# Kernel optimization log

Hardware: AMD Instinct MI355X
Metric: run time of the kernel (lower is better)

The kernel has to match this reference:

```python
import jax, jax.numpy as jnp
import numpy as np

N, E, DIN, H, C = 50000, 800000, 128, 2, 64  # C = hidden_dim*heads (per-head out channels); concat=False -> mean over heads -> layer out dim C
NUM_CLASSES = 4
EPS_GN = 1e-5


def setup_inputs() -> dict:
    key = jax.random.key(0)

    def rn(i, shape, scale):
        return (jax.random.normal(jax.random.fold_in(key, i), shape) * scale).astype(jnp.float32)

    inp = {
        "x": rn(0, (N, DIN), 1.0),
        "edge_index": jax.random.randint(jax.random.fold_in(key, 1), (2, E), 0, N, dtype=jnp.int32),
    }
    layer_in = [DIN, C]
    for li, din in enumerate(layer_in, 1):
        s = 1.0 / np.sqrt(din)
        base = 10 * li
        inp[f"Wl{li}"] = rn(base + 0, (din, H * C), s)
        inp[f"bl{li}"] = jnp.zeros((H * C,), jnp.float32)
        inp[f"Wr{li}"] = rn(base + 1, (din, H * C), s)
        inp[f"br{li}"] = jnp.zeros((H * C,), jnp.float32)
        inp[f"att{li}"] = rn(base + 2, (H, C), 1.0 / np.sqrt(C))
        inp[f"bias{li}"] = jnp.zeros((C,), jnp.float32)
        inp[f"gng{li}"] = jnp.ones((C,), jnp.float32)   # GraphNorm weight
        inp[f"gnb{li}"] = jnp.zeros((C,), jnp.float32)  # GraphNorm bias
        inp[f"gna{li}"] = jnp.ones((C,), jnp.float32)   # GraphNorm mean_scale
    inp["W1"] = rn(100, (C, NUM_CLASSES), 1.0 / np.sqrt(C))
    inp["b1"] = jnp.zeros((NUM_CLASSES,), jnp.float32)
    return inp


def gatv2_layer(x, src, dst, Wl, bl, Wr, br, att, bias):
    # PyG GATv2Conv, concat=False. x: [N, din]
    n = x.shape[0]
    xl = (x @ Wl + bl).reshape(n, H, C)  # source transform
    xr = (x @ Wr + br).reshape(n, H, C)  # target transform
    m = jax.nn.leaky_relu(xl[src] + xr[dst], negative_slope=0.2)  # [E', H, C]
    e = jnp.einsum('ehc,hc->eh', m, att)                           # [E', H]
    emax = jax.lax.stop_gradient(jax.ops.segment_max(e, dst, num_segments=n))
    ee = jnp.exp(e - emax[dst])
    denom = jax.ops.segment_sum(ee, dst, num_segments=n)
    alpha = ee / (denom[dst] + 1e-16)                              # softmax over in-edges of each target
    out = jax.ops.segment_sum(alpha[:, :, None] * xl[src], dst, num_segments=n)  # [N, H, C]
    return out.mean(axis=1) + bias  # concat=False -> mean over heads


def graph_norm(x, gamma, beta, mean_scale):
    # single-graph GraphNorm: stats over all nodes, per feature
    mean = x.mean(axis=0, keepdims=True)
    xc = x - mean_scale * mean
    var = (xc * xc).mean(axis=0, keepdims=True)
    return gamma * xc * jax.lax.rsqrt(var + EPS_GN) + beta


def reference(x, edge_index,
              Wl1, bl1, Wr1, br1, att1, bias1, gng1, gnb1, gna1,
              Wl2, bl2, Wr2, br2, att2, bias2, gng2, gnb2, gna2,
              W1, b1):
    src, dst = edge_index[0], edge_index[1]
    loops = jnp.arange(N, dtype=src.dtype)  # add_self_loops=True
    src = jnp.concatenate([src, loops])
    dst = jnp.concatenate([dst, loops])

    h = gatv2_layer(x, src, dst, Wl1, bl1, Wr1, br1, att1, bias1)
    h = graph_norm(h, gng1, gnb1, gna1)
    h = gatv2_layer(h, src, dst, Wl2, bl2, Wr2, br2, att2, bias2)
    h = graph_norm(h, gng2, gnb2, gna2)

    logits = h @ W1 + b1  # dropout is identity in eval
    return jax.nn.log_softmax(logits, axis=1)
```

## Files before the change

kernel.cpp:

```cpp
#include <hip/hip_runtime.h>
#include <hip/hip_bf16.h>
#include <math.h>

#define HC   128
#define CCH  64
#define NBK  256

typedef __attribute__((ext_vector_type(8))) short short8;
typedef __attribute__((ext_vector_type(4))) float floatx4;

__device__ __forceinline__ unsigned short f2bf(float f) {
  unsigned u = __float_as_uint(f);
  u += 0x7fffu + ((u >> 16) & 1u);
  return (unsigned short)(u >> 16);
}

__device__ __forceinline__ void unpack8(uint4 u, float* f) {
  f[0] = __uint_as_float(u.x << 16);
  f[1] = __uint_as_float(u.x & 0xffff0000u);
  f[2] = __uint_as_float(u.y << 16);
  f[3] = __uint_as_float(u.y & 0xffff0000u);
  f[4] = __uint_as_float(u.z << 16);
  f[5] = __uint_as_float(u.z & 0xffff0000u);
  f[6] = __uint_as_float(u.w << 16);
  f[7] = __uint_as_float(u.w & 0xffff0000u);
}

template <int CTRL>
__device__ __forceinline__ float dpp_add(float x) {
  int t = __builtin_amdgcn_update_dpp(0, __float_as_int(x), CTRL, 0xf, 0xf, true);
  return x + __int_as_float(t);
}

template <int K>
__device__ __forceinline__ void gemm32rows(
    const unsigned short* __restrict__ A,
    const unsigned short* __restrict__ Wlt, const unsigned short* __restrict__ Wrt,
    const float* __restrict__ bl, const float* __restrict__ br,
    unsigned short* __restrict__ xlb, unsigned short* __restrict__ xrb,
    int M, int row0, int tid) {
  const int w = tid >> 6;
  const int lane = tid & 63;
  const bool isR = w >= 2;
  const unsigned short* Wt = isR ? Wrt : Wlt;
  const float* bias = isR ? br : bl;
  unsigned short* out = isR ? xrb : xlb;
  const int col0 = (w & 1) * 64;
  const int mrow = lane & 15, quad = lane >> 4;
  const unsigned short* pa0 = A + (size_t)(row0 + mrow) * K + quad * 8;
  const unsigned short* pa1 = pa0 + (size_t)16 * K;
  const unsigned short* pb = Wt + (size_t)(col0 + mrow) * K + quad * 8;
  floatx4 acc[2][4];
#pragma unroll
  for (int gp = 0; gp < 2; gp++)
#pragma unroll
    for (int ct = 0; ct < 4; ct++) acc[gp][ct] = (floatx4){0.f, 0.f, 0.f, 0.f};
#pragma unroll
  for (int k0 = 0; k0 < K; k0 += 32) {
    short8 a0 = *(const short8*)(pa0 + k0);
    short8 a1 = *(const short8*)(pa1 + k0);
    short8 b0 = *(const short8*)(pb + k0);
    short8 b1 = *(const short8*)(pb + 16 * K + k0);
    short8 b2 = *(const short8*)(pb + 32 * K + k0);
    short8 b3 = *(const short8*)(pb + 48 * K + k0);
    acc[0][0] = __builtin_amdgcn_mfma_f32_16x16x32_bf16(a0, b0, acc[0][0], 0, 0, 0);
    acc[1][0] = __builtin_amdgcn_mfma_f32_16x16x32_bf16(a1, b0, acc[1][0], 0, 0, 0);
    acc[0][1] = __builtin_amdgcn_mfma_f32_16x16x32_bf16(a0, b1, acc[0][1], 0, 0, 0);
    acc[1][1] = __builtin_amdgcn_mfma_f32_16x16x32_bf16(a1, b1, acc[1][1], 0, 0, 0);
    acc[0][2] = __builtin_amdgcn_mfma_f32_16x16x32_bf16(a0, b2, acc[0][2], 0, 0, 0);
    acc[1][2] = __builtin_amdgcn_mfma_f32_16x16x32_bf16(a1, b2, acc[1][2], 0, 0, 0);
    acc[0][3] = __builtin_amdgcn_mfma_f32_16x16x32_bf16(a0, b3, acc[0][3], 0, 0, 0);
    acc[1][3] = __builtin_amdgcn_mfma_f32_16x16x32_bf16(a1, b3, acc[1][3], 0, 0, 0);
  }
#pragma unroll
  for (int gp = 0; gp < 2; gp++) {
#pragma unroll
    for (int ct = 0; ct < 4; ct++) {
      int col = col0 + ct * 16 + mrow;
      float bv = bias[col];
#pragma unroll
      for (int r = 0; r < 4; r++) {
        int row = row0 + gp * 16 + quad * 4 + r;
        if (row < M) out[(size_t)row * HC + col] = f2bf(acc[gp][ct][r] + bv);
      }
    }
  }
}

__global__ __launch_bounds__(256) void bin_cast(
    const int* __restrict__ ei, int E, int chunk, int nB,
    int* __restrict__ blkCnt, int* __restrict__ bucketTotal,
    const float* __restrict__ x, unsigned short* __restrict__ xb, int cnt4,
    const float* __restrict__ Wl, const float* __restrict__ Wr,
    unsigned short* __restrict__ Wlt, unsigned short* __restrict__ Wrt) {
  if ((int)blockIdx.x < NBK) {
    __shared__ int cnt[512];
    for (int j = threadIdx.x; j < nB; j += 256) cnt[j] = 0;
    __syncthreads();
    int e0 = blockIdx.x * chunk;
    int e1 = e0 + chunk; e1 = e1 < E ? e1 : E;
    int e = e0 + threadIdx.x;
    for (; e + 768 < e1; e += 1024) {
      int d0 = __builtin_nontemporal_load(ei + E + e);
      int d1 = __builtin_nontemporal_load(ei + E + e + 256);
      int d2 = __builtin_nontemporal_load(ei + E + e + 512);
      int d3 = __builtin_nontemporal_load(ei + E + e + 768);
      atomicAdd(&cnt[d0 >> 7], 1);
      atomicAdd(&cnt[d1 >> 7], 1);
      atomicAdd(&cnt[d2 >> 7], 1);
      atomicAdd(&cnt[d3 >> 7], 1);
    }
    for (; e < e1; e += 256) {
      int dst = __builtin_nontemporal_load(ei + E + e);
      atomicAdd(&cnt[dst >> 7], 1);
    }
    __syncthreads();
    for (int j = threadIdx.x; j < nB; j += 256) {
      int c = cnt[j];
      blkCnt[blockIdx.x * nB + j] = c;
      if (c) atomicAdd(&bucketTotal[j], c);
    }
  } else {
    int gid = (blockIdx.x - NBK) * 256 + threadIdx.x;
    if (gid < 32768) {
      int sel = gid >> 14;
      int i = gid & 16383;
      int nn = i >> 7, k = i & 127;
      const float* W = sel ? Wr : Wl;
      unsigned short* Wt = sel ? Wrt : Wlt;
      Wt[i] = f2bf(W[k * HC + nn]);
    }
    if (gid >= cnt4) return;
    float4 v = ((const float4*)x)[gid];
    ushort4 o;
    o.x = f2bf(v.x); o.y = f2bf(v.y); o.z = f2bf(v.z); o.w = f2bf(v.w);
    ((ushort4*)xb)[gid] = o;
  }
}

__global__ __launch_bounds__(256) void scan_offsets(
    const int* __restrict__ bucketTotal, int* __restrict__ bucketBase,
    int* __restrict__ blkCnt, int nB, int E) {
  const int j = blockIdx.x;
  const int tid = threadIdx.x;
  __shared__ int red[256];
  __shared__ int col[NBK];
  int s = 0;
  for (int k = tid; k < j; k += 256) s += bucketTotal[k];
  red[tid] = s;
  __syncthreads();
  for (int off = 128; off > 0; off >>= 1) {
    if (tid < off) red[tid] += red[tid + off];
    __syncthreads();
  }
  const int base_j = red[0];
  if (tid == 0) {
    bucketBase[j] = base_j;
    if (j == 0) bucketBase[nB] = E;
  }
  int v = 0;
  if (tid < NBK) { v = blkCnt[tid * nB + j]; col[tid] = v; }
  __syncthreads();
  for (int off = 1; off < NBK; off <<= 1) {
    int t = 0;
    if (tid < NBK && tid >= off) t = col[tid - off];
    __syncthreads();
    if (tid < NBK) col[tid] += t;
    __syncthreads();
  }
  if (tid < NBK) blkCnt[tid * nB + j] = base_j + col[tid] - v;
}

__global__ __launch_bounds__(256) void place_gemm1(
    const int* __restrict__ ei, int E, int chunk, int nB,
    const int* __restrict__ blkCnt, unsigned* __restrict__ ebuf,
    const unsigned short* __restrict__ A,
    const unsigned short* __restrict__ Wlt, const unsigned short* __restrict__ Wrt,
    const float* __restrict__ bl, const float* __restrict__ br,
    unsigned short* __restrict__ xlb, unsigned short* __restrict__ xrb, int M) {
  if ((int)blockIdx.x < NBK) {
    __shared__ int cur[512];
    for (int j = threadIdx.x; j < nB; j += 256)
      cur[j] = blkCnt[blockIdx.x * nB + j];
    __syncthreads();
    int e0 = blockIdx.x * chunk;
    int e1 = e0 + chunk; e1 = e1 < E ? e1 : E;
    int e = e0 + threadIdx.x;
    for (; e + 768 < e1; e += 1024) {
      int d0 = __builtin_nontemporal_load(ei + E + e);
      int d1 = __builtin_nontemporal_load(ei + E + e + 256);
      int d2 = __builtin_nontemporal_load(ei + E + e + 512);
      int d3 = __builtin_nontemporal_load(ei + E + e + 768);
      int s0 = __builtin_nontemporal_load(ei + e);
      int s1 = __builtin_nontemporal_load(ei + e + 256);
      int s2 = __builtin_nontemporal_load(ei + e + 512);
      int s3 = __builtin_nontemporal_load(ei + e + 768);
      int p0 = atomicAdd(&cur[d0 >> 7], 1);
      int p1 = atomicAdd(&cur[d1 >> 7], 1);
      int p2 = atomicAdd(&cur[d2 >> 7], 1);
      int p3 = atomicAdd(&cur[d3 >> 7], 1);
      ebuf[p0] = (unsigned)s0 | ((unsigned)(d0 & 127) << 16);
      ebuf[p1] = (unsigned)s1 | ((unsigned)(d1 & 127) << 16);
      ebuf[p2] = (unsigned)s2 | ((unsigned)(d2 & 127) << 16);
      ebuf[p3] = (unsigned)s3 | ((unsigned)(d3 & 127) << 16);
    }
    for (; e < e1; e += 256) {
      int dst = __builtin_nontemporal_load(ei + E + e);
      int src = __builtin_nontemporal_load(ei + e);
      int pos = atomicAdd(&cur[dst >> 7], 1);
      ebuf[pos] = (unsigned)src | ((unsigned)(dst & 127) << 16);
    }
  } else {
    const int row0 = (blockIdx.x - NBK) * 32;
    if (row0 >= M) return;
    gemm32rows<128>(A, Wlt, Wrt, bl, br, xlb, xrb, M, row0, threadIdx.x);
  }
}

__global__ __launch_bounds__(256) void csr_build(
    const unsigned* __restrict__ ebuf, const int* __restrict__ bucketBase,
    int* __restrict__ row_start, int* __restrict__ deg,
    int* __restrict__ csr_src, int N, int EPtot) {
  const int b = blockIdx.x;
  const int tid = threadIdx.x;
  const int node0 = b * 128;
  const int nb = (N - node0) < 128 ? (N - node0) : 128;
  const int ebase = bucketBase[b];
  const int eend = bucketBase[b + 1];
  __shared__ int degL[128], scanL[128], curL[128];
  if (tid < 128) degL[tid] = 0;
  __syncthreads();
  for (int e = ebase + tid; e < eend; e += 256)
    atomicAdd(&degL[(ebuf[e] >> 16) & 127], 1);
  __syncthreads();
  if (tid < 128) scanL[tid] = degL[tid];
  __syncthreads();
  for (int off = 1; off < 128; off <<= 1) {
    int t = 0;
    if (tid < 128 && tid >= off) t = scanL[tid - off];
    __syncthreads();
    if (tid < 128) scanL[tid] += t;
    __syncthreads();
  }
  if (tid < 128) {
    int rs = ebase + (scanL[tid] - degL[tid]) + node0 + tid;
    curL[tid] = rs;
    if (tid < nb) {
      row_start[node0 + tid] = rs;
      deg[node0 + tid] = degL[tid];
    }
  }
  __syncthreads();
  for (int e = ebase + tid; e < eend; e += 256) {
    unsigned p = ebuf[e];
    int pos = atomicAdd(&curL[(p >> 16) & 127], 1);
    csr_src[pos] = (int)(p & 0xffffu);
  }
  __syncthreads();
  if (tid < nb) csr_src[curL[tid]] = node0 + tid;
  if (b == 0 && tid < 32) csr_src[EPtot + tid] = 0;
}

template <int K>
__global__ __launch_bounds__(256) void gemm_mfma(
    const unsigned short* __restrict__ A,
    const unsigned short* __restrict__ Wlt, const unsigned short* __restrict__ Wrt,
    const float* __restrict__ bl, const float* __restrict__ br,
    unsigned short* __restrict__ xlb, unsigned short* __restrict__ xrb, int M) {
  const int row0 = blockIdx.x * 32;
  if (row0 >= M) return;
  gemm32rows<K>(A, Wlt, Wrt, bl, br, xlb, xrb, M, row0, threadIdx.x);
}

__global__ __launch_bounds__(256) void node_attn(
    const unsigned short* __restrict__ xlb, const unsigned short* __restrict__ xrb,
    const int* __restrict__ csr_src, const int* __restrict__ row_start,
    const int* __restrict__ deg, const float* __restrict__ att,
    const float* __restrict__ bias, unsigned short* __restrict__ outb, int n) {
  int wave = (blockIdx.x * blockDim.x + threadIdx.x) >> 6;
  if (wave >= n) return;
  const int node = wave;
  const int lane = threadIdx.x & 63;
  const int g = lane >> 4;
  const int hl = lane & 15;
  const int c8 = hl << 3;

  float r[8], a[8];
  {
    uint4 u = *(const uint4*)(xrb + (size_t)node * HC + c8);
    unpack8(u, r);
    float4 a0 = *(const float4*)(att + c8);
    float4 a1 = *(const float4*)(att + c8 + 4);
    const float L2E = 1.44269504f;
    a[0] = a0.x * L2E; a[1] = a0.y * L2E; a[2] = a0.z * L2E; a[3] = a0.w * L2E;
    a[4] = a1.x * L2E; a[5] = a1.y * L2E; a[6] = a1.z * L2E; a[7] = a1.w * L2E;
  }

  const int p0 = row_start[node];
  const int pend = p0 + deg[node] + 1;

  float d = 0.f;
  float acc[8] = {0.f, 0.f, 0.f, 0.f, 0.f, 0.f, 0.f, 0.f};

  int s0 = __builtin_nontemporal_load(csr_src + p0 + g);
  uint4 A0 = *(const uint4*)(xlb + (size_t)s0 * HC + c8);
  int s1 = __builtin_nontemporal_load(csr_src + p0 + 4 + g);
  uint4 A1 = *(const uint4*)(xlb + (size_t)s1 * HC + c8);
  int s2 = __builtin_nontemporal_load(csr_src + p0 + 8 + g);
  uint4 A2 = *(const uint4*)(xlb + (size_t)s2 * HC + c8);

  for (int p = p0; p < pend; p += 4) {
    int s3 = __builtin_nontemporal_load(csr_src + p + 12 + g);
    uint4 A3 = *(const uint4*)(xlb + (size_t)s3 * HC + c8);

    float v[8];
    unpack8(A0, v);
    float e1 = 0.f, e2 = 0.f;
#pragma unroll
    for (int i = 0; i < 8; i++) {
      float s = v[i] + r[i];
      e1 = fmaf(a[i], s, e1);
      e2 = fmaf(a[i], fabsf(s), e2);
    }
    float e = fmaf(0.4f, e2, 0.6f * e1);
    e = dpp_add<0xB1>(e);
    e = dpp_add<0x4E>(e);
    e = dpp_add<0x141>(e);

    bool valid = (p + g) < pend;
    float w = valid ? exp2f(e) : 0.f;
    d += w;
#pragma unroll
    for (int i = 0; i < 8; i++) acc[i] = fmaf(w, v[i], acc[i]);
    A0 = A1; A1 = A2; A2 = A3;
  }

#pragma unroll
  for (int ofs = 16; ofs <= 32; ofs <<= 1) {
    d += __shfl_xor(d, ofs);
#pragma unroll
    for (int i = 0; i < 8; i++) acc[i] += __shfl_xor(acc[i], ofs);
  }
  float inv = 1.f / (d + 1e-16f);
  const float* bb = bias + (c8 & 63);
  float o[8];
#pragma unroll
  for (int i = 0; i < 8; i++) {
    float t = acc[i] * inv;
    float t2 = __shfl_xor(t, 8);
    o[i] = 0.5f * (t + t2) + bb[i];
  }
  if (lane < 8) {
    uint4 ou;
    ou.x = (unsigned)f2bf(o[0]) | ((unsigned)f2bf(o[1]) << 16);
    ou.y = (unsigned)f2bf(o[2]) | ((unsigned)f2bf(o[3]) << 16);
    ou.z = (unsigned)f2bf(o[4]) | ((unsigned)f2bf(o[5]) << 16);
    ou.w = (unsigned)f2bf(o[6]) | ((unsigned)f2bf(o[7]) << 16);
    *(uint4*)(outb + (size_t)node * CCH + c8) = ou;
  }
}

__global__ __launch_bounds__(256) void gn_stats(
    const unsigned short* __restrict__ y, float* __restrict__ S, int n) {
  __shared__ float l1a[256], l1b[256], l2a[256], l2b[256];
  int half = threadIdx.x & 31;
  int sub = threadIdx.x >> 5;
  float s1a = 0.f, s1b = 0.f, s2a = 0.f, s2b = 0.f;
  int stride = gridDim.x * 8;
  for (int r = blockIdx.x * 8 + sub; r < n; r += stride) {
    unsigned u = ((const unsigned*)(y + (size_t)r * CCH))[half];
    float va = __uint_as_float(u << 16);
    float vb = __uint_as_float(u & 0xffff0000u);
    s1a += va; s2a = fmaf(va, va, s2a);
    s1b += vb; s2b = fmaf(vb, vb, s2b);
  }
  l1a[threadIdx.x] = s1a; l1b[threadIdx.x] = s1b;
  l2a[threadIdx.x] = s2a; l2b[threadIdx.x] = s2b;
  __syncthreads();
  if (threadIdx.x < 32) {
#pragma unroll
    for (int k = 1; k < 8; k++) {
      s1a += l1a[threadIdx.x + 32 * k];
      s1b += l1b[threadIdx.x + 32 * k];
      s2a += l2a[threadIdx.x + 32 * k];
      s2b += l2b[threadIdx.x + 32 * k];
    }
    atomicAdd(&S[2 * half], s1a);
    atomicAdd(&S[2 * half + 1], s1b);
    atomicAdd(&S[64 + 2 * half], s2a);
    atomicAdd(&S[64 + 2 * half + 1], s2b);
  }
}

__global__ __launch_bounds__(256) void gn_stats_prep(
    const unsigned short* __restrict__ y, float* __restrict__ S,
    int* __restrict__ done, const float* __restrict__ gamma,
    const float* __restrict__ beta, const float* __restrict__ mscale,
    const float* __restrict__ Wl2, const float* __restrict__ bl2,
    const float* __restrict__ Wr2, const float* __restrict__ br2,
    unsigned short* __restrict__ Wl2tb, float* __restrict__ bl2p,
    unsigned short* __restrict__ Wr2tb, float* __restrict__ br2p, int n) {
  __shared__ float l1a[256], l1b[256], l2a[256], l2b[256];
  int half = threadIdx.x & 31;
  int sub = threadIdx.x >> 5;
  float s1a = 0.f, s1b = 0.f, s2a = 0.f, s2b = 0.f;
  int stride = gridDim.x * 8;
  for (int r = blockIdx.x * 8 + sub; r < n; r += stride) {
    unsigned u = ((const unsigned*)(y + (size_t)r * CCH))[half];
    float va = __uint_as_float(u << 16);
    float vb = __uint_as_float(u & 0xffff0000u);
    s1a += va; s2a = fmaf(va, va, s2a);
    s1b += vb; s2b = fmaf(vb, vb, s2b);
  }
  l1a[threadIdx.x] = s1a; l1b[threadIdx.x] = s1b;
  l2a[threadIdx.x] = s2a; l2b[threadIdx.x] = s2b;
  __syncthreads();
  if (threadIdx.x < 32) {
#pragma unroll
    for (int k = 1; k < 8; k++) {
      s1a += l1a[threadIdx.x + 32 * k];
      s1b += l1b[threadIdx.x + 32 * k];
      s2a += l2a[threadIdx.x + 32 * k];
      s2b += l2b[threadIdx.x + 32 * k];
    }
    atomicAdd(&S[2 * half], s1a);
    atomicAdd(&S[2 * half + 1], s1b);
    atomicAdd(&S[64 + 2 * half], s2a);
    atomicAdd(&S[64 + 2 * half + 1], s2b);
  }
  __threadfence();
  __shared__ int isLast;
  if (threadIdx.x == 0) {
    int old = atomicAdd(done, 1);
    isLast = (old == (int)gridDim.x - 1) ? 1 : 0;
  }
  __syncthreads();
  if (!isLast) return;
  __threadfence();
  __shared__ float As[64], Bs[64];
  int t = threadIdx.x;
  if (t < 64) {
    float invn = 1.f / (float)n;
    float mu = S[t] * invn;
    float ms = mscale[t];
    float var = S[64 + t] * invn - 2.f * ms * mu * mu + ms * ms * mu * mu;
    float A = gamma[t] * rsqrtf(var + 1e-5f);
    As[t] = A;
    Bs[t] = beta[t] - A * ms * mu;
  }
  __syncthreads();
  const int side = t >> 7, col = t & 127;
  const float* W = side ? Wr2 : Wl2;
  unsigned short* Wt = side ? Wr2tb : Wl2tb;
  const float* bin = side ? br2 : bl2;
  float* bout = side ? br2p : bl2p;
  float s = 0.f;
  for (int c = 0; c < 64; c++) {
    float w = W[c * HC + col];
    Wt[col * 64 + c] = f2bf(As[c] * w);
    s = fmaf(Bs[c], w, s);
  }
  bout[col] = bin[col] + s;
}

__global__ __launch_bounds__(256) void classify(
    const unsigned short* __restrict__ h,
    const float* __restrict__ S, const float* __restrict__ gamma,
    const float* __restrict__ beta, const float* __restrict__ mscale,
    const float* __restrict__ W, const float* __restrict__ b,
    float* __restrict__ out, int n) {
  __shared__ float4 sW[64];
  __shared__ float sBt[256];
  __shared__ float sb[4];
  int tid = threadIdx.x;
  if (tid < 64) {
    float invn = 1.f / (float)n;
    float mu = S[tid] * invn;
    float ms = mscale[tid];
    float var = S[64 + tid] * invn - 2.f * ms * mu * mu + ms * ms * mu * mu;
    float A = gamma[tid] * rsqrtf(var + 1e-5f);
    float B = beta[tid] - A * ms * mu;
    float4 w = ((const float4*)W)[tid];
    sW[tid] = make_float4(A * w.x, A * w.y, A * w.z, A * w.w);
    sBt[tid * 4 + 0] = B * w.x; sBt[tid * 4 + 1] = B * w.y;
    sBt[tid * 4 + 2] = B * w.z; sBt[tid * 4 + 3] = B * w.w;
  }
  __syncthreads();
  if (tid < 4) {
    float s = b[tid];
    for (int c = 0; c < 64; c++) s += sBt[c * 4 + tid];
    sb[tid] = s;
  }
  __syncthreads();
  int node = blockIdx.x * 256 + tid;
  if (node >= n) return;
  float acc0 = sb[0], acc1 = sb[1], acc2 = sb[2], acc3 = sb[3];
  const uint4* row = (const uint4*)(h + (size_t)node * CCH);
#pragma unroll
  for (int k4 = 0; k4 < 8; k4++) {
    uint4 u = row[k4];
    float v[8];
    unpack8(u, v);
#pragma unroll
    for (int j = 0; j < 8; j++) {
      float4 w = sW[k4 * 8 + j];
      acc0 = fmaf(v[j], w.x, acc0);
      acc1 = fmaf(v[j], w.y, acc1);
      acc2 = fmaf(v[j], w.z, acc2);
      acc3 = fmaf(v[j], w.w, acc3);
    }
  }
  float mx = fmaxf(fmaxf(acc0, acc1), fmaxf(acc2, acc3));
  float s = __expf(acc0 - mx) + __expf(acc1 - mx) + __expf(acc2 - mx) + __expf(acc3 - mx);
  float lse = mx + logf(s);
  float4 o = make_float4(acc0 - lse, acc1 - lse, acc2 - lse, acc3 - lse);
  *((float4*)(out + (size_t)node * 4)) = o;
}

extern "C" void kernel_launch(void* const* d_in, const int* in_sizes, int n_in,
                              void* d_out, int out_size, void* d_ws, size_t ws_size,
                              hipStream_t stream) {
  const float* x     = (const float*)d_in[0];
  const int*   ei    = (const int*)d_in[1];
  const float* Wl1   = (const float*)d_in[2];
  const float* bl1   = (const float*)d_in[3];
  const float* Wr1   = (const float*)d_in[4];
  const float* br1   = (const float*)d_in[5];
  const float* att1  = (const float*)d_in[6];
  const float* bias1 = (const float*)d_in[7];
  const float* gng1  = (const float*)d_in[8];
  const float* gnb1  = (const float*)d_in[9];
  const float* gna1  = (const float*)d_in[10];
  const float* Wl2   = (const float*)d_in[11];
  const float* bl2   = (const float*)d_in[12];
  const float* Wr2   = (const float*)d_in[13];
  const float* br2   = (const float*)d_in[14];
  const float* att2  = (const float*)d_in[15];
  const float* bias2 = (const float*)d_in[16];
  const float* gng2  = (const float*)d_in[17];
  const float* gnb2  = (const float*)d_in[18];
  const float* gna2  = (const float*)d_in[19];
  const float* W1    = (const float*)d_in[20];
  const float* b1    = (const float*)d_in[21];

  const int N = in_sizes[0] / 128;
  const int E = in_sizes[1] / 2;
  const int EP = E + N;
  const int nB = (N + 127) >> 7;
  const int chunk = (E + NBK - 1) / NBK;

  int* bucketTotal = (int*)d_ws;
  float* S1  = (float*)(bucketTotal + 512);
  float* S2  = S1 + 128;
  int* done  = (int*)(S2 + 128);
  float* bl2p = (float*)(done + 64);
  float* br2p = bl2p + 128;
  unsigned short* xb    = (unsigned short*)(br2p + 128);
  unsigned short* xlb   = xb + (size_t)N * HC;
  unsigned short* xrb   = xlb + (size_t)N * HC;
  unsigned short* aggb  = xrb + (size_t)N * HC;
  unsigned short* Wl1tb = aggb + (size_t)N * CCH;
  unsigned short* Wr1tb = Wl1tb + HC * HC;
  unsigned short* Wl2tb = Wr1tb + HC * HC;
  unsigned short* Wr2tb = Wl2tb + HC * CCH;
  int* bucketBase = (int*)(Wr2tb + HC * CCH);
  int* blkCnt  = bucketBase + 512 + 8;
  int* row_st  = blkCnt + NBK * 512;
  int* deg     = row_st + N;
  unsigned* ebuf = (unsigned*)(deg + N);
  int* csr_src = (int*)(ebuf + E);

  dim3 b256(256);
  const int gNode = (N * 64 + 255) / 256;
  const int gCls  = (N + 255) / 256;
  const int gCast = (N * 32 + 255) / 256;
  const int gGemm = (N + 31) / 32;

  hipMemsetAsync(d_ws, 0, 4096, stream);

  bin_cast<<<NBK + gCast, b256, 0, stream>>>(
      ei, E, chunk, nB, blkCnt, bucketTotal,
      x, xb, N * 32, Wl1, Wr1, Wl1tb, Wr1tb);

  scan_offsets<<<nB, b256, 0, stream>>>(bucketTotal, bucketBase, blkCnt, nB, E);

  place_gemm1<<<NBK + gGemm, b256, 0, stream>>>(
      ei, E, chunk, nB, blkCnt, ebuf,
      xb, Wl1tb, Wr1tb, bl1, br1, xlb, xrb, N);

  csr_build<<<nB, b256, 0, stream>>>(ebuf, bucketBase, row_st, deg, csr_src, N, EP);

  node_attn<<<gNode, b256, 0, stream>>>(xlb, xrb, csr_src, row_st, deg, att1, bias1, aggb, N);
  gn_stats_prep<<<256, b256, 0, stream>>>(aggb, S1, done, gng1, gnb1, gna1,
                                          Wl2, bl2, Wr2, br2,
                                          Wl2tb, bl2p, Wr2tb, br2p, N);

  gemm_mfma<64><<<gGemm, b256, 0, stream>>>(aggb, Wl2tb, Wr2tb, bl2p, br2p, xlb, xrb, N);
  node_attn<<<gNode, b256, 0, stream>>>(xlb, xrb, csr_src, row_st, deg, att2, bias2, aggb, N);
  gn_stats<<<256, b256, 0, stream>>>(aggb, S2, N);

  classify<<<gCls, b256, 0, stream>>>(aggb, S2, gng2, gnb2, gna2, W1, b1,
                                      (float*)d_out, N);
}
```

Before: 327.0 us.

## Merge edge binning and placement into one pass with fixed-capacity buckets

Edge bucketing now reserves each block's slots per bucket with a global atomicAdd right after the local count, then places edges into fixed-capacity per-bucket regions within the same kernel. This removes the separate offset-scan kernel and lets the CSR build run alongside the first GEMM in one launch, cutting the pipeline from four launches to two. Each CSR block computes its own global base by summing the bucket counts before it. The cost is a second read of edge_index in the binning kernel, plain cached loads instead of nontemporal ones, and a fixed capacity of twice the average bucket size, which would overflow silently on skewed degree distributions.

```diff
diff --git a/kernel.cpp b/kernel.cpp
--- a/kernel.cpp
+++ b/kernel.cpp
@@ -4,7 +4,7 @@
 
 #define HC   128
 #define CCH  64
-#define NBK  256
+#define NBKE 256
 
 typedef __attribute__((ext_vector_type(8))) short short8;
 typedef __attribute__((ext_vector_type(4))) float floatx4;
@@ -87,13 +87,13 @@
   }
 }
 
-__global__ __launch_bounds__(256) void bin_cast(
-    const int* __restrict__ ei, int E, int chunk, int nB,
-    int* __restrict__ blkCnt, int* __restrict__ bucketTotal,
+__global__ __launch_bounds__(256) void binplace_cast(
+    const int* __restrict__ ei, int E, int chunk, int nB, int cap,
+    int* __restrict__ gCnt, unsigned* __restrict__ ebuf,
     const float* __restrict__ x, unsigned short* __restrict__ xb, int cnt4,
     const float* __restrict__ Wl, const float* __restrict__ Wr,
     unsigned short* __restrict__ Wlt, unsigned short* __restrict__ Wrt) {
-  if ((int)blockIdx.x < NBK) {
+  if ((int)blockIdx.x < NBKE) {
     __shared__ int cnt[512];
     for (int j = threadIdx.x; j < nB; j += 256) cnt[j] = 0;
     __syncthreads();
@@ -101,27 +101,50 @@
     int e1 = e0 + chunk; e1 = e1 < E ? e1 : E;
     int e = e0 + threadIdx.x;
     for (; e + 768 < e1; e += 1024) {
-      int d0 = __builtin_nontemporal_load(ei + E + e);
-      int d1 = __builtin_nontemporal_load(ei + E + e + 256);
-      int d2 = __builtin_nontemporal_load(ei + E + e + 512);
-      int d3 = __builtin_nontemporal_load(ei + E + e + 768);
+      int d0 = ei[E + e];
+      int d1 = ei[E + e + 256];
+      int d2 = ei[E + e + 512];
+      int d3 = ei[E + e + 768];
       atomicAdd(&cnt[d0 >> 7], 1);
       atomicAdd(&cnt[d1 >> 7], 1);
       atomicAdd(&cnt[d2 >> 7], 1);
       atomicAdd(&cnt[d3 >> 7], 1);
     }
-    for (; e < e1; e += 256) {
-      int dst = __builtin_nontemporal_load(ei + E + e);
-      atomicAdd(&cnt[dst >> 7], 1);
-    }
+    for (; e < e1; e += 256) atomicAdd(&cnt[ei[E + e] >> 7], 1);
     __syncthreads();
     for (int j = threadIdx.x; j < nB; j += 256) {
       int c = cnt[j];
-      blkCnt[blockIdx.x * nB + j] = c;
-      if (c) atomicAdd(&bucketTotal[j], c);
+      int base = c ? atomicAdd(&gCnt[j], c) : 0;
+      cnt[j] = j * cap + base;
+    }
+    __syncthreads();
+    e = e0 + threadIdx.x;
+    for (; e + 768 < e1; e += 1024) {
+      int d0 = ei[E + e];
+      int d1 = ei[E + e + 256];
+      int d2 = ei[E + e + 512];
+      int d3 = ei[E + e + 768];
+      int s0 = ei[e];
+      int s1 = ei[e + 256];
+      int s2 = ei[e + 512];
+      int s3 = ei[e + 768];
+      int p0 = atomicAdd(&cnt[d0 >> 7], 1);
+      int p1 = atomicAdd(&cnt[d1 >> 7], 1);
+      int p2 = atomicAdd(&cnt[d2 >> 7], 1);
+      int p3 = atomicAdd(&cnt[d3 >> 7], 1);
+      ebuf[p0] = (unsigned)s0 | ((unsigned)(d0 & 127) << 16);
+      ebuf[p1] = (unsigned)s1 | ((unsigned)(d1 & 127) << 16);
+      ebuf[p2] = (unsigned)s2 | ((unsigned)(d2 & 127) << 16);
+      ebuf[p3] = (unsigned)s3 | ((unsigned)(d3 & 127) << 16);
+    }
+    for (; e < e1; e += 256) {
+      int dst = ei[E + e];
+      int src = ei[e];
+      int pos = atomicAdd(&cnt[dst >> 7], 1);
+      ebuf[pos] = (unsigned)src | ((unsigned)(dst & 127) << 16);
     }
   } else {
-    int gid = (blockIdx.x - NBK) * 256 + threadIdx.x;
+    int gid = (blockIdx.x - NBKE) * 256 + threadIdx.x;
     if (gid < 32768) {
       int sel = gid >> 14;
       int i = gid & 16383;
@@ -138,127 +161,68 @@
   }
 }
 
-__global__ __launch_bounds__(256) void scan_offsets(
-    const int* __restrict__ bucketTotal, int* __restrict__ bucketBase,
-    int* __restrict__ blkCnt, int nB, int E) {
-  const int j = blockIdx.x;
-  const int tid = threadIdx.x;
-  __shared__ int red[256];
-  __shared__ int col[NBK];
-  int s = 0;
-  for (int k = tid; k < j; k += 256) s += bucketTotal[k];
-  red[tid] = s;
-  __syncthreads();
-  for (int off = 128; off > 0; off >>= 1) {
-    if (tid < off) red[tid] += red[tid + off];
-    __syncthreads();
-  }
-  const int base_j = red[0];
-  if (tid == 0) {
-    bucketBase[j] = base_j;
-    if (j == 0) bucketBase[nB] = E;
-  }
-  int v = 0;
-  if (tid < NBK) { v = blkCnt[tid * nB + j]; col[tid] = v; }
-  __syncthreads();
-  for (int off = 1; off < NBK; off <<= 1) {
-    int t = 0;
-    if (tid < NBK && tid >= off) t = col[tid - off];
-    __syncthreads();
-    if (tid < NBK) col[tid] += t;
-    __syncthreads();
-  }
-  if (tid < NBK) blkCnt[tid * nB + j] = base_j + col[tid] - v;
-}
-
-__global__ __launch_bounds__(256) void place_gemm1(
-    const int* __restrict__ ei, int E, int chunk, int nB,
-    const int* __restrict__ blkCnt, unsigned* __restrict__ ebuf,
+__global__ __launch_bounds__(256) void csr_gemm1(
+    const unsigned* __restrict__ ebuf, const int* __restrict__ gCnt, int cap,
+    int* __restrict__ row_start, int* __restrict__ deg,
+    int* __restrict__ csr_src, int N, int EPtot, int nB,
     const unsigned short* __restrict__ A,
     const unsigned short* __restrict__ Wlt, const unsigned short* __restrict__ Wrt,
     const float* __restrict__ bl, const float* __restrict__ br,
     unsigned short* __restrict__ xlb, unsigned short* __restrict__ xrb, int M) {
-  if ((int)blockIdx.x < NBK) {
-    __shared__ int cur[512];
-    for (int j = threadIdx.x; j < nB; j += 256)
-      cur[j] = blkCnt[blockIdx.x * nB + j];
-    __syncthreads();
-    int e0 = blockIdx.x * chunk;
-    int e1 = e0 + chunk; e1 = e1 < E ? e1 : E;
-    int e = e0 + threadIdx.x;
-    for (; e + 768 < e1; e += 1024) {
-      int d0 = __builtin_nontemporal_load(ei + E + e);
-      int d1 = __builtin_nontemporal_load(ei + E + e + 256);
-      int d2 = __builtin_nontemporal_load(ei + E + e + 512);
-      int d3 = __builtin_nontemporal_load(ei + E + e + 768);
-      int s0 = __builtin_nontemporal_load(ei + e);
-      int s1 = __builtin_nontemporal_load(ei + e + 256);
-      int s2 = __builtin_nontemporal_load(ei + e + 512);
-      int s3 = __builtin_nontemporal_load(ei + e + 768);
-      int p0 = atomicAdd(&cur[d0 >> 7], 1);
-      int p1 = atomicAdd(&cur[d1 >> 7], 1);
-      int p2 = atomicAdd(&cur[d2 >> 7], 1);
-      int p3 = atomicAdd(&cur[d3 >> 7], 1);
-      ebuf[p0] = (unsigned)s0 | ((unsigned)(d0 & 127) << 16);
-      ebuf[p1] = (unsigned)s1 | ((unsigned)(d1 & 127) << 16);
-      ebuf[p2] = (unsigned)s2 | ((unsigned)(d2 & 127) << 16);
-      ebuf[p3] = (unsigned)s3 | ((unsigned)(d3 & 127) << 16);
-    }
-    for (; e < e1; e += 256) {
-      int dst = __builtin_nontemporal_load(ei + E + e);
-      int src = __builtin_nontemporal_load(ei + e);
-      int pos = atomicAdd(&cur[dst >> 7], 1);
-      ebuf[pos] = (unsigned)src | ((unsigned)(dst & 127) << 16);
-    }
+  if ((int)blockIdx.x < nB) {
+    const int b = blockIdx.x;
+    const int tid = threadIdx.x;
+    __shared__ int red[256];
+    __shared__ int degL[128], scanL[128], curL[128];
+    int s = 0;
+    for (int k = tid; k < b; k += 256) s += gCnt[k];
+    red[tid] = s;
+    __syncthreads();
+    for (int off = 128; off > 0; off >>= 1) {
+      if (tid < off) red[tid] += red[tid + off];
+      __syncthreads();
+    }
+    const int ebase = red[0];
+    const int cnt = gCnt[b];
+    const int node0 = b * 128;
+    const int nb2 = (N - node0) < 128 ? (N - node0) : 128;
+    const unsigned* eb = ebuf + (size_t)b * cap;
+    if (tid < 128) degL[tid] = 0;
+    __syncthreads();
+    for (int e = tid; e < cnt; e += 256)
+      atomicAdd(&degL[(eb[e] >> 16) & 127], 1);
+    __syncthreads();
+    if (tid < 128) scanL[tid] = degL[tid];
+    __syncthreads();
+    for (int off = 1; off < 128; off <<= 1) {
+      int t = 0;
+      if (tid < 128 && tid >= off) t = scanL[tid - off];
+      __syncthreads();
+      if (tid < 128) scanL[tid] += t;
+      __syncthreads();
+    }
+    if (tid < 128) {
+      int rs = ebase + (scanL[tid] - degL[tid]) + node0 + tid;
+      curL[tid] = rs;
+      if (tid < nb2) {
+        row_start[node0 + tid] = rs;
+        deg[node0 + tid] = degL[tid];
+      }
+    }
+    __syncthreads();
+    for (int e = tid; e < cnt; e += 256) {
+      unsigned p = eb[e];
+      int pos = atomicAdd(&curL[(p >> 16) & 127], 1);
+      csr_src[pos] = (int)(p & 0xffffu);
+    }
+    __syncthreads();
+    if (tid < nb2) csr_src[curL[tid]] = node0 + tid;
+    if (b == 0 && tid < 32) csr_src[EPtot + tid] = 0;
   } else {
-    const int row0 = (blockIdx.x - NBK) * 32;
+    const int row0 = (blockIdx.x - nB) * 32;
     if (row0 >= M) return;
     gemm32rows<128>(A, Wlt, Wrt, bl, br, xlb, xrb, M, row0, threadIdx.x);
   }
-}
-
-__global__ __launch_bounds__(256) void csr_build(
-    const unsigned* __restrict__ ebuf, const int* __restrict__ bucketBase,
-    int* __restrict__ row_start, int* __restrict__ deg,
-    int* __restrict__ csr_src, int N, int EPtot) {
-  const int b = blockIdx.x;
-  const int tid = threadIdx.x;
-  const int node0 = b * 128;
-  const int nb = (N - node0) < 128 ? (N - node0) : 128;
-  const int ebase = bucketBase[b];
-  const int eend = bucketBase[b + 1];
-  __shared__ int degL[128], scanL[128], curL[128];
-  if (tid < 128) degL[tid] = 0;
-  __syncthreads();
-  for (int e = ebase + tid; e < eend; e += 256)
-    atomicAdd(&degL[(ebuf[e] >> 16) & 127], 1);
-  __syncthreads();
-  if (tid < 128) scanL[tid] = degL[tid];
-  __syncthreads();
-  for (int off = 1; off < 128; off <<= 1) {
-    int t = 0;
-    if (tid < 128 && tid >= off) t = scanL[tid - off];
-    __syncthreads();
-    if (tid < 128) scanL[tid] += t;
-    __syncthreads();
-  }
-  if (tid < 128) {
-    int rs = ebase + (scanL[tid] - degL[tid]) + node0 + tid;
-    curL[tid] = rs;
-    if (tid < nb) {
-      row_start[node0 + tid] = rs;
-      deg[node0 + tid] = degL[tid];
-    }
-  }
-  __syncthreads();
-  for (int e = ebase + tid; e < eend; e += 256) {
-    unsigned p = ebuf[e];
-    int pos = atomicAdd(&curL[(p >> 16) & 127], 1);
-    csr_src[pos] = (int)(p & 0xffffu);
-  }
-  __syncthreads();
-  if (tid < nb) csr_src[curL[tid]] = node0 + tid;
-  if (b == 0 && tid < 32) csr_src[EPtot + tid] = 0;
 }
 
 template <int K>
@@ -547,10 +511,11 @@
   const int E = in_sizes[1] / 2;
   const int EP = E + N;
   const int nB = (N + 127) >> 7;
-  const int chunk = (E + NBK - 1) / NBK;
-
-  int* bucketTotal = (int*)d_ws;
-  float* S1  = (float*)(bucketTotal + 512);
+  const int chunk = (E + NBKE - 1) / NBKE;
+  const int cap = ((E / nB) * 2 + 255) & ~255;
+
+  int* gCnt = (int*)d_ws;
+  float* S1  = (float*)(gCnt + 512);
   float* S2  = S1 + 128;
   int* done  = (int*)(S2 + 128);
   float* bl2p = (float*)(done + 64);
@@ -563,12 +528,10 @@
   unsigned short* Wr1tb = Wl1tb + HC * HC;
   unsigned short* Wl2tb = Wr1tb + HC * HC;
   unsigned short* Wr2tb = Wl2tb + HC * CCH;
-  int* bucketBase = (int*)(Wr2tb + HC * CCH);
-  int* blkCnt  = bucketBase + 512 + 8;
-  int* row_st  = blkCnt + NBK * 512;
+  int* row_st  = (int*)(Wr2tb + HC * CCH);
   int* deg     = row_st + N;
   unsigned* ebuf = (unsigned*)(deg + N);
-  int* csr_src = (int*)(ebuf + E);
+  int* csr_src = (int*)(ebuf + (size_t)nB * cap);
 
   dim3 b256(256);
   const int gNode = (N * 64 + 255) / 256;
@@ -578,17 +541,13 @@
 
   hipMemsetAsync(d_ws, 0, 4096, stream);
 
-  bin_cast<<<NBK + gCast, b256, 0, stream>>>(
-      ei, E, chunk, nB, blkCnt, bucketTotal,
+  binplace_cast<<<NBKE + gCast, b256, 0, stream>>>(
+      ei, E, chunk, nB, cap, gCnt, ebuf,
       x, xb, N * 32, Wl1, Wr1, Wl1tb, Wr1tb);
 
-  scan_offsets<<<nB, b256, 0, stream>>>(bucketTotal, bucketBase, blkCnt, nB, E);
-
-  place_gemm1<<<NBK + gGemm, b256, 0, stream>>>(
-      ei, E, chunk, nB, blkCnt, ebuf,
+  csr_gemm1<<<nB + gGemm, b256, 0, stream>>>(
+      ebuf, gCnt, cap, row_st, deg, csr_src, N, EP, nB,
       xb, Wl1tb, Wr1tb, bl1, br1, xlb, xrb, N);
-
-  csr_build<<<nB, b256, 0, stream>>>(ebuf, bucketBase, row_st, deg, csr_src, N, EP);
 
   node_attn<<<gNode, b256, 0, stream>>>(xlb, xrb, csr_src, row_st, deg, att1, bias1, aggb, N);
   gn_stats_prep<<<256, b256, 0, stream>>>(aggb, S1, done, gng1, gnb1, gna1,
```

Measured after the change: 316.5 us. -3.2%, faster.
